# Performance work log

Measured on AMD Instinct MI355X. Metric: run time of the kernel, lower is better.

Reference implementation:

```python
import jax, jax.numpy as jnp
import numpy as np

B, N, T, NUM_API = 4, 160, 512, 20000  # queries, list length, tag vocab size, number of APIs
TAG_DENSITY = 0.05


def _compute_lambda(y_score, tag_set, M):
    # y_score: [N]; tag_set: [N,T] multi-hot rows api_tag_embedding[y_pred]; M: [T] multi-hot target.
    # Faithful to mode == 'cover' branch of LambdaRankLoss.compute_lambda.
    n = tag_set.shape[0]
    f32 = tag_set.dtype
    idx = jnp.arange(n)
    log_values = jnp.log2(jnp.arange(2, n + 2, dtype=f32))             # [N]
    P = jax.lax.cummax(tag_set, axis=0)                                # set_union_list = cummax(tag_set) [N,T]
    Mc = (jnp.count_nonzero(M) + 1).astype(f32)                        # M_nonzero_count
    # count_nonzero(clamp(M - set_union_list[k], min=0)) == #(M_t > P[k,t])
    cU = jnp.sum(M[None, :] > P, axis=1).astype(f32)                   # [N]

    # pre[i] = rowwise-max of tag_set[:i-1]. Torch quirk: i==0 -> tag_set[:-1] (all but last row); i==1 -> empty.
    pre = jnp.where(idx[:, None] == 0, P[n - 2][None, :],
                    jnp.where(idx[:, None] == 1, jnp.zeros((), f32),
                              P[jnp.clip(idx - 2, 0, n - 1)]))         # [N,T] (0 is max-identity: entries >= 0)

    # R[a,b] = max(tag_set[a..b]) along rows; 0 when b < a (rows before a masked to 0, then cummax)
    masked = jnp.where(idx[None, :, None] >= idx[:, None, None], tag_set[None, :, :], jnp.zeros((), f32))
    R = jax.lax.cummax(masked, axis=1)                                 # [N,N,T]

    # mid[k,i] = max(tag_set[i+1:k]) = R[i+1, k-1] when k >= i+2, else empty -> 0
    i_ix = idx[None, :]
    k_ix = idx[:, None]
    mid = jnp.where((k_ix >= i_ix + 2)[:, :, None],
                    R[jnp.clip(i_ix + 1, 0, n - 1), jnp.clip(k_ix - 1, 0, n - 1)],
                    jnp.zeros((), f32))                                # [K,I,T]

    # A[k,i] = max(cat(tag_set[:i-1], tag_set[i+1:k]));  Q[k,i,j] = max(A[k,i], tag_set[j])
    A = jnp.maximum(pre[None, :, :], mid)                              # [K,I,T]
    # count_nonzero(clamp(M - Q[k,i,j], 0)) = sum_t [M_t > A[k,i,t]] * [M_t > tag_set[j,t]]
    aM = (M[None, None, :] > A).astype(f32)                            # [K,I,T]
    bM = (M[None, :] > tag_set).astype(f32)                            # [J,T]
    cQ = jnp.einsum('kit,jt->kij', aM, bM)                             # [K,I,J] Q_nonzero counts

    W = (cU[:, None, None] - cQ) / (Mc * log_values[:, None, None])    # [K,I,J]
    # Z1[i,j] = sum_{k=i}^{j-1} W[k,i,j]  (strictly upper-triangular in (i,j))
    maskZ = (idx[None, :, None] <= idx[:, None, None]) & (idx[:, None, None] < idx[None, None, :])
    Z1 = jnp.sum(jnp.where(maskZ, W, jnp.zeros((), f32)), axis=0)      # [I,J]

    # lambda1[i,j] = 1 / (1 + exp(s_i - s_j))
    lam = 1.0 / (1.0 + jnp.exp(y_score[:, None] - y_score[None, :]))
    return jnp.sum(lam * Z1) / jnp.asarray(n + 1, f32)


def setup_inputs() -> dict:
    key = jax.random.key(0)
    k1, k2, k3, k4 = jax.random.split(key, 4)
    y_scores = jax.random.normal(k1, (B, N), jnp.float32)
    y_preds = jax.random.randint(k2, (B, N), 0, NUM_API)
    M = (jax.random.uniform(k3, (B, T)) < TAG_DENSITY).astype(jnp.float32)
    api_tag_embedding = (jax.random.uniform(k4, (NUM_API, T)) < TAG_DENSITY).astype(jnp.float32)
    return {"y_scores": y_scores, "M": M, "api_tag_embedding": api_tag_embedding, "y_preds": y_preds}


def reference(y_scores, M, api_tag_embedding, y_preds):
    def per_query(s, m, pred):
        return _compute_lambda(s, api_tag_embedding[pred], m)
    vals = jax.vmap(per_query)(y_scores, M, y_preds)  # [B]
    return jnp.mean(vals)  # loss / len(y_scores)
```

## Files before the change

kernel.cpp:

```cpp
#include <hip/hip_runtime.h>
#include <stdint.h>

typedef unsigned long long u64;

constexpr int B_ = 4;
constexpr int N_ = 160;
constexpr int T_ = 512;
constexpr int W_ = T_ / 64;

__global__ __launch_bounds__(64) void pack_tags(const float* __restrict__ emb,
                                                const int* __restrict__ preds,
                                                u64* __restrict__ tags) {
    int row  = blockIdx.x;
    int lane = threadIdx.x;
    const float* src = emb + (long long)preds[row] * T_;
#pragma unroll
    for (int w = 0; w < W_; ++w) {
        float v = src[w * 64 + lane];
        u64 m = __ballot(v != 0.0f);
        if (lane == 0) tags[(long long)row * W_ + w] = m;
    }
}

__global__ __launch_bounds__(256) void pack_scan(const float* __restrict__ Mf,
                                                 const u64* __restrict__ tags,
                                                 u64* __restrict__ Mp,
                                                 u64* __restrict__ P,
                                                 float* __restrict__ cU,
                                                 float* __restrict__ Mc) {
    __shared__ u64 S0[N_ * W_];
    __shared__ u64 S1[N_ * W_];
    __shared__ u64 Msh[W_];

    const int b    = blockIdx.x;
    const int tid  = threadIdx.x;
    const int lane = tid & 63;
    const int wv   = tid >> 6;

    for (int w = wv; w < W_; w += 4) {
        float v = Mf[(long long)b * T_ + w * 64 + lane];
        u64 m = __ballot(v != 0.0f);
        if (lane == 0) { Msh[w] = m; Mp[b * W_ + w] = m; }
    }
    for (int x = tid; x < N_ * W_; x += 256)
        S0[x] = tags[(long long)b * N_ * W_ + x];
    __syncthreads();

    u64* src = S0;
    u64* dst = S1;
    for (int d = 1; d < N_; d <<= 1) {
        for (int x = tid; x < N_ * W_; x += 256) {
            int r = x >> 3;
            u64 v = src[x];
            if (r >= d) v |= src[x - d * W_];
            dst[x] = v;
        }
        __syncthreads();
        u64* t = src; src = dst; dst = t;
    }

    for (int x = tid; x < N_ * W_; x += 256)
        P[(long long)b * N_ * W_ + x] = src[x];

    if (tid < N_) {
        int c = 0;
#pragma unroll
        for (int w = 0; w < W_; ++w)
            c += __popcll(Msh[w] & ~src[tid * W_ + w]);
        cU[b * N_ + tid] = (float)c;
    }
    if (tid == 0) {
        int c = 0;
#pragma unroll
        for (int w = 0; w < W_; ++w) c += __popcll(Msh[w]);
        Mc[b] = (float)(c + 1);
    }
}

__global__ __launch_bounds__(192) void lambda_main(const u64* __restrict__ tags,
                                                   const u64* __restrict__ Mp,
                                                   const u64* __restrict__ P,
                                                   const float* __restrict__ cU,
                                                   const float* __restrict__ Mc,
                                                   const float* __restrict__ scores,
                                                   double* __restrict__ partials) {
    __shared__ u64 tagsL[N_ * W_];
    __shared__ float cUL[N_];
    __shared__ float invlogL[N_];
    __shared__ float scoresL[N_];
    __shared__ float redF[3];

    const int i   = blockIdx.x;
    const int b   = blockIdx.y;
    const int tid = threadIdx.x;

    for (int x = tid; x < N_ * W_; x += blockDim.x)
        tagsL[x] = tags[(long long)b * N_ * W_ + x];
    for (int x = tid; x < N_; x += blockDim.x) {
        cUL[x]     = cU[b * N_ + x];
        scoresL[x] = scores[b * N_ + x];
        invlogL[x] = 1.0f / log2f((float)(x + 2));
    }
    __syncthreads();

    u64 Mw[W_], aw[W_];
#pragma unroll
    for (int w = 0; w < W_; ++w) Mw[w] = Mp[b * W_ + w];
    if (i == 1) {
#pragma unroll
        for (int w = 0; w < W_; ++w) aw[w] = Mw[w];
    } else {
        int src = (i == 0) ? (N_ - 2) : (i - 2);
#pragma unroll
        for (int w = 0; w < W_; ++w)
            aw[w] = Mw[w] & ~P[((long long)b * N_ + src) * W_ + w];
    }

    const int j = tid;
    u64 Bw[W_];
    float lam = 0.0f;
    if (j < N_) {
#pragma unroll
        for (int w = 0; w < W_; ++w) Bw[w] = Mw[w] & ~tagsL[j * W_ + w];
        lam = 1.0f / (1.0f + __expf(scoresL[i] - scoresL[j]));
    }

    float acc = 0.0f;
    for (int k = i; k <= N_ - 2; ++k) {
        if (k >= i + 2) {
#pragma unroll
            for (int w = 0; w < W_; ++w) aw[w] &= ~tagsL[(k - 1) * W_ + w];
        }
        if (j > k && j < N_) {
            int c = 0;
#pragma unroll
            for (int w = 0; w < W_; ++w) c += __popcll(aw[w] & Bw[w]);
            acc += invlogL[k] * (cUL[k] - (float)c);
        }
    }

    float val = (j < N_) ? lam * acc : 0.0f;
    for (int off = 32; off >= 1; off >>= 1) val += __shfl_down(val, off, 64);
    if ((tid & 63) == 0) redF[tid >> 6] = val;
    __syncthreads();
    if (tid == 0) {
        float s = redF[0] + redF[1] + redF[2];
        partials[b * N_ + i] = (double)s / (double)Mc[b];
    }
}

__global__ __launch_bounds__(256) void finalize(const double* __restrict__ partials,
                                                float* __restrict__ out) {
    __shared__ double redD[4];
    const int tid = threadIdx.x;
    double s = 0.0;
    for (int x = tid; x < B_ * N_; x += 256) s += partials[x];
    for (int off = 32; off >= 1; off >>= 1) s += __shfl_down(s, off, 64);
    if ((tid & 63) == 0) redD[tid >> 6] = s;
    __syncthreads();
    if (tid == 0) {
        double t = redD[0] + redD[1] + redD[2] + redD[3];
        out[0] = (float)(t / ((double)(N_ + 1) * (double)B_));
    }
}

extern "C" void kernel_launch(void* const* d_in, const int* in_sizes, int n_in,
                              void* d_out, int out_size, void* d_ws, size_t ws_size,
                              hipStream_t stream) {
    const float* y_scores = (const float*)d_in[0];
    const float* Mf       = (const float*)d_in[1];
    const float* emb      = (const float*)d_in[2];
    const int*   preds    = (const int*)d_in[3];
    float* out = (float*)d_out;

    u64* tags = (u64*)d_ws;
    u64* P    = tags + (size_t)B_ * N_ * W_;
    u64* Mp   = P + (size_t)B_ * N_ * W_;
    double* partials = (double*)(Mp + B_ * W_);
    float* cU = (float*)(partials + B_ * N_);
    float* Mc = cU + B_ * N_;

    pack_tags<<<B_ * N_, 64, 0, stream>>>(emb, preds, tags);
    pack_scan<<<B_, 256, 0, stream>>>(Mf, tags, Mp, P, cU, Mc);
    dim3 grid(N_, B_);
    lambda_main<<<grid, 192, 0, stream>>>(tags, Mp, P, cU, Mc, y_scores, partials);
    finalize<<<1, 256, 0, stream>>>(partials, out);
}
```

Baseline: 134.7 us.

## Parallelize lambda kernel over k with per-block suffix-OR scan and flattened (i,j) pairs

Each block now handles one list position k instead of one i. It builds suffix ORs of the tag rows before k with an in-shared-memory log-step scan, forms the A and B masks in transposed shared layout, and distributes all (i,j) pairs with i<=k<j evenly across 256 threads. This replaces the old serial loop over k per thread, which left work imbalanced across blocks and threads. The cost is nine scan passes with barriers per block, plus five shared arrays of about 10KB each, which may lower occupancy.

```diff
diff --git a/kernel.cpp b/kernel.cpp
--- a/kernel.cpp
+++ b/kernel.cpp
@@ -77,75 +77,103 @@
     }
 }
 
-__global__ __launch_bounds__(192) void lambda_main(const u64* __restrict__ tags,
+__global__ __launch_bounds__(256) void lambda_main(const u64* __restrict__ tags,
                                                    const u64* __restrict__ Mp,
                                                    const u64* __restrict__ P,
                                                    const float* __restrict__ cU,
                                                    const float* __restrict__ Mc,
                                                    const float* __restrict__ scores,
                                                    double* __restrict__ partials) {
-    __shared__ u64 tagsL[N_ * W_];
-    __shared__ float cUL[N_];
-    __shared__ float invlogL[N_];
+    constexpr int LD = N_ + 1;
+    __shared__ u64 tagsT[W_ * LD];
+    __shared__ u64 bufA[W_ * LD];
+    __shared__ u64 bufB[W_ * LD];
+    __shared__ u64 awT[W_ * LD];
+    __shared__ u64 bT[W_ * LD];
+    __shared__ u64 Msh[W_];
     __shared__ float scoresL[N_];
-    __shared__ float redF[3];
-
-    const int i   = blockIdx.x;
+    __shared__ float redF[4];
+
+    const int k   = blockIdx.x;
     const int b   = blockIdx.y;
     const int tid = threadIdx.x;
 
-    for (int x = tid; x < N_ * W_; x += blockDim.x)
-        tagsL[x] = tags[(long long)b * N_ * W_ + x];
-    for (int x = tid; x < N_; x += blockDim.x) {
-        cUL[x]     = cU[b * N_ + x];
-        scoresL[x] = scores[b * N_ + x];
-        invlogL[x] = 1.0f / log2f((float)(x + 2));
-    }
-    __syncthreads();
-
-    u64 Mw[W_], aw[W_];
-#pragma unroll
-    for (int w = 0; w < W_; ++w) Mw[w] = Mp[b * W_ + w];
-    if (i == 1) {
-#pragma unroll
-        for (int w = 0; w < W_; ++w) aw[w] = Mw[w];
-    } else {
-        int src = (i == 0) ? (N_ - 2) : (i - 2);
-#pragma unroll
-        for (int w = 0; w < W_; ++w)
-            aw[w] = Mw[w] & ~P[((long long)b * N_ + src) * W_ + w];
-    }
-
-    const int j = tid;
-    u64 Bw[W_];
-    float lam = 0.0f;
-    if (j < N_) {
-#pragma unroll
-        for (int w = 0; w < W_; ++w) Bw[w] = Mw[w] & ~tagsL[j * W_ + w];
-        lam = 1.0f / (1.0f + __expf(scoresL[i] - scoresL[j]));
-    }
-
-    float acc = 0.0f;
-    for (int k = i; k <= N_ - 2; ++k) {
-        if (k >= i + 2) {
-#pragma unroll
-            for (int w = 0; w < W_; ++w) aw[w] &= ~tagsL[(k - 1) * W_ + w];
-        }
-        if (j > k && j < N_) {
-            int c = 0;
-#pragma unroll
-            for (int w = 0; w < W_; ++w) c += __popcll(aw[w] & Bw[w]);
-            acc += invlogL[k] * (cUL[k] - (float)c);
-        }
-    }
-
-    float val = (j < N_) ? lam * acc : 0.0f;
+    if (tid < W_)  Msh[tid]    = Mp[b * W_ + tid];
+    if (tid < N_)  scoresL[tid] = scores[b * N_ + tid];
+
+    for (int x = tid; x < W_ * N_; x += 256) {
+        int r = x >> 3, w = x & 7;
+        tagsT[w * LD + r] = tags[(long long)b * N_ * W_ + x];
+    }
+    __syncthreads();
+
+    for (int x = tid; x < W_ * N_; x += 256) {
+        int r = x >> 3, w = x & 7;
+        bufA[w * LD + r] = (r < k) ? tagsT[w * LD + r] : 0ull;
+    }
+    __syncthreads();
+
+    u64* src = bufA;
+    u64* dst = bufB;
+    for (int d = 1; d < N_; d <<= 1) {
+        for (int x = tid; x < W_ * N_; x += 256) {
+            int r = x >> 3, w = x & 7;
+            u64 v = src[w * LD + r];
+            if (r + d < k) v |= src[w * LD + r + d];
+            dst[w * LD + r] = v;
+        }
+        __syncthreads();
+        u64* t = src; src = dst; dst = t;
+    }
+
+    for (int x = tid; x < W_ * N_; x += 256) {
+        int i = x >> 3, w = x & 7;
+        u64 pre;
+        if (i == 1) pre = 0ull;
+        else {
+            int sr = (i == 0) ? (N_ - 2) : (i - 2);
+            pre = P[((long long)b * N_ + sr) * W_ + w];
+        }
+        u64 sv = (i + 1 < k) ? src[w * LD + i + 1] : 0ull;
+        awT[w * LD + i] = Msh[w] & ~pre & ~sv;
+        bT[w * LD + i]  = Msh[w] & ~tagsT[w * LD + i];
+    }
+    __syncthreads();
+
+    const int m = N_ - 1 - k;
+    float accLam = 0.0f, accC = 0.0f;
+    if (m > 0) {
+        const int npairs = (k + 1) * m;
+        if (tid < npairs) {
+            int cnt = (npairs - tid + 255) >> 8;
+            int i   = tid / m;
+            int jj  = tid - i * m;
+            const int di = 256 / m;
+            const int rj = 256 - di * m;
+            for (int c = 0; c < cnt; ++c) {
+                const int j = k + 1 + jj;
+                int cc = 0;
+#pragma unroll
+                for (int w = 0; w < W_; ++w)
+                    cc += __popcll(awT[w * LD + i] & bT[w * LD + j]);
+                float lam = 1.0f / (1.0f + __expf(scoresL[i] - scoresL[j]));
+                accLam += lam;
+                accC   += lam * (float)cc;
+                i += di; jj += rj;
+                if (jj >= m) { jj -= m; ++i; }
+            }
+        }
+    }
+
+    const float cUk = cU[b * N_ + k];
+    float val = cUk * accLam - accC;
     for (int off = 32; off >= 1; off >>= 1) val += __shfl_down(val, off, 64);
     if ((tid & 63) == 0) redF[tid >> 6] = val;
     __syncthreads();
     if (tid == 0) {
-        float s = redF[0] + redF[1] + redF[2];
-        partials[b * N_ + i] = (double)s / (double)Mc[b];
+        float s = redF[0] + redF[1] + redF[2] + redF[3];
+        float invlog = 1.0f / log2f((float)(k + 2));
+        partials[b * N_ + k] = (double)(s * invlog) / (double)Mc[b];
     }
 }
 
@@ -183,6 +211,6 @@
     pack_tags<<<B_ * N_, 64, 0, stream>>>(emb, preds, tags);
     pack_scan<<<B_, 256, 0, stream>>>(Mf, tags, Mp, P, cU, Mc);
     dim3 grid(N_, B_);
-    lambda_main<<<grid, 192, 0, stream>>>(tags, Mp, P, cU, Mc, y_scores, partials);
+    lambda_main<<<grid, 256, 0, stream>>>(tags, Mp, P, cU, Mc, y_scores, partials);
     finalize<<<1, 256, 0, stream>>>(partials, out);
 }
```

Result: faster. 113.1 us (-16.0%).
